# Performance work log

Hardware: AMD Instinct MI355X
Metric: run time of the kernel (lower is better)

The kernel has to match this reference:

```python
import jax, jax.numpy as jnp
import numpy as np

DEPTH = 24
D_MODEL = 384
D_INNER = 768          # expand=2.0
D_STATE = 16
DT_RANK = 24           # ceil(384/16)
D_CONV = 3
PATCH = 16
IMG = 224
N_PATCH = (IMG // PATCH) ** 2  # 196
BATCH = 4


def setup_inputs() -> dict:
    key = jax.random.key(0)
    ks = jax.random.split(key, 12)
    f = lambda k, shape, s=0.02: (jax.random.normal(k, shape) * s).astype(jnp.float32)
    # S4D-real init for A_log, as in mamba
    A_log = jnp.log(jnp.tile(jnp.arange(1, D_STATE + 1, dtype=jnp.float32), (DEPTH, D_INNER, 1)))
    dt_bias = jnp.full((DEPTH, D_INNER), float(np.log(np.expm1(0.01))), dtype=jnp.float32)
    return {
        "z": jax.random.normal(ks[0], (BATCH, 3, IMG, IMG), jnp.float32),
        "x": jax.random.normal(ks[1], (BATCH, 3, IMG, IMG), jnp.float32),
        "patch_W": f(ks[2], (D_MODEL, 3, PATCH, PATCH)),
        "patch_b": jnp.zeros((D_MODEL,), jnp.float32),
        "pos_embed": f(ks[3], (1, N_PATCH + 1, D_MODEL)),
        "norm_w": jnp.ones((DEPTH, D_MODEL), jnp.float32),
        "norm_b": jnp.zeros((DEPTH, D_MODEL), jnp.float32),
        "in_W": f(ks[4], (DEPTH, 2 * D_INNER, D_MODEL)),
        "conv_W": f(ks[5], (DEPTH, D_INNER, D_CONV), 0.2),
        "conv_b": jnp.zeros((DEPTH, D_INNER), jnp.float32),
        "xproj_W": f(ks[6], (DEPTH, DT_RANK + 2 * D_STATE, D_INNER)),
        "dtproj_W": f(ks[7], (DEPTH, D_INNER, DT_RANK), 0.1),
        "dtproj_b": dt_bias,
        "A_log": A_log,
        "D_param": jnp.ones((DEPTH, D_INNER), jnp.float32),
        "out_W": f(ks[8], (DEPTH, D_MODEL, D_INNER)),
        "fnorm_w": jnp.ones((D_MODEL,), jnp.float32),
        "fnorm_b": jnp.zeros((D_MODEL,), jnp.float32),
    }


def _layernorm(x, w, b):
    mu = jnp.mean(x, axis=-1, keepdims=True)
    var = jnp.var(x, axis=-1, keepdims=True)
    return (x - mu) * jax.lax.rsqrt(var + 1e-5) * w + b


def _mixer(x, iw, cw, cb, xw, dw, db, al, dd, ow):
    # x: (B, L, d_model)
    B_, L, _ = x.shape
    xz = jnp.einsum('bld,ed->ble', x, iw)            # (B, L, 2*d_inner)
    xs, zg = jnp.split(xz, 2, axis=-1)
    # depthwise causal conv1d along L (kernel D_CONV)
    xp = jnp.pad(xs, ((0, 0), (D_CONV - 1, 0), (0, 0)))
    xc = cb + sum(xp[:, j:j + L, :] * cw[:, j] for j in range(D_CONV))
    xc = jax.nn.silu(xc)
    dbl = jnp.einsum('bld,ed->ble', xc, xw)          # (B, L, dt_rank + 2*N)
    dt = dbl[..., :DT_RANK]
    Bm = dbl[..., DT_RANK:DT_RANK + D_STATE]         # (B, L, N)
    Cm = dbl[..., DT_RANK + D_STATE:]                # (B, L, N)
    dt = jax.nn.softplus(jnp.einsum('blr,dr->bld', dt, dw) + db)  # (B, L, d_inner)
    A = -jnp.exp(al)                                  # (d_inner, N)
    dA = jnp.exp(dt[..., None] * A)                   # (B, L, d_inner, N)
    dBu = (dt * xc)[..., None] * Bm[:, :, None, :]    # (B, L, d_inner, N)

    def step(h, inp):
        dA_t, dBu_t, C_t = inp
        h = dA_t * h + dBu_t
        return h, jnp.einsum('bdn,bn->bd', h, C_t)

    h0 = jnp.zeros((B_, D_INNER, D_STATE), x.dtype)
    _, ys = jax.lax.scan(step, h0, (dA.transpose(1, 0, 2, 3), dBu.transpose(1, 0, 2, 3), Cm.transpose(1, 0, 2)))
    y = ys.transpose(1, 0, 2) + dd * xc               # (B, L, d_inner)
    y = y * jax.nn.silu(zg)
    return jnp.einsum('ble,de->bld', y, ow)           # (B, L, d_model)


def reference(z, x, patch_W, patch_b, pos_embed, norm_w, norm_b, in_W, conv_W, conv_b,
              xproj_W, dtproj_W, dtproj_b, A_log, D_param, out_W, fnorm_w, fnorm_b):
    def embed(img):
        feat = jax.lax.conv_general_dilated(img, patch_W, (PATCH, PATCH), 'VALID',
                                            dimension_numbers=('NCHW', 'OIHW', 'NCHW'))
        B_, C, H, W = feat.shape
        feat = feat.reshape(B_, C, H * W).transpose(0, 2, 1) + patch_b  # (B, 196, d)
        return feat + pos_embed[:, 1:, :]

    h = jnp.concatenate([embed(z), embed(x)], axis=1)  # (B, 392, d)

    def block(carry, p):
        nw, nb, iw, cw, cb, xw, dw, db, al, dd, ow = p
        y = _layernorm(carry, nw, nb)
        y = _mixer(y, iw, cw, cb, xw, dw, db, al, dd, ow)
        return carry + y, None

    h, _ = jax.lax.scan(block, h, (norm_w, norm_b, in_W, conv_W, conv_b, xproj_W,
                                   dtproj_W, dtproj_b, A_log, D_param, out_W))
    return _layernorm(h, fnorm_w, fnorm_b)
```

## Files before the change

kernel.cpp:

```cpp
#include <hip/hip_runtime.h>

typedef unsigned short u16;
typedef unsigned int   u32;

#define B_     4
#define L_     392
#define T_     1568
#define DM     384
#define DI     768
#define DS     16
#define DTR    24
#define DEPTH_ 24
#define NPATCH 196
#define NC     28
#define CL     14

#define XKC    96
#define XPAD   104
#define OKC    384
#define OPAD   392

typedef __bf16 bf16x8 __attribute__((ext_vector_type(8)));
typedef float  f32x4  __attribute__((ext_vector_type(4)));
typedef u16    u16x4  __attribute__((ext_vector_type(4)));
typedef u16    u16x8  __attribute__((ext_vector_type(8)));

__device__ __forceinline__ u16 f2bf(float f) {
  union { float f; u32 u; } v; v.f = f;
  return (u16)((v.u + 0x7fffu + ((v.u >> 16) & 1u)) >> 16);
}
__device__ __forceinline__ float bf2f(u16 h) {
  union { u32 u; float f; } v; v.u = (u32)h << 16; return v.f;
}

#define RQ0 36864
#define RQ1 1769472
#define RQ2 147456
#define RQ3 884736
#define RQ4 43904
#define RQ_TOT (RQ0+RQ1+RQ2+RQ3+RQ4)

__global__ __launch_bounds__(256) void repack_kernel(
    const float* __restrict__ patchW, u16* __restrict__ pwB,
    const float* __restrict__ inW,    u16* __restrict__ inWb,
    const float* __restrict__ xpW,    u16* __restrict__ xpWb,
    const float* __restrict__ outW,   u16* __restrict__ outWb,
    float* __restrict__ dblz) {
  int i = blockIdx.x * 256 + threadIdx.x;
  const float* sp = nullptr; u16* dp = nullptr;
  if (i < RQ0) {
    int r = i & 15, kb = (i >> 4) % 96, p = i / (16 * 96);
    sp = patchW + (size_t)(p * 16 + r) * 768 + kb * 8;
    dp = pwB + (size_t)i * 8;
  } else { i -= RQ0;
  if (i < RQ1) {
    const int per = 1536 * 48;
    int ly = i / per, rem = i - ly * per;
    int r = rem & 15, kb = (rem >> 4) % 48, p = rem / (16 * 48);
    sp = inW + (size_t)ly * 1536 * 384 + (size_t)(p * 16 + r) * 384 + kb * 8;
    dp = inWb + (size_t)i * 8;
  } else { i -= RQ1;
  if (i < RQ2) {
    const int per = 64 * 96;
    int ly = i / per, rem = i - ly * per;
    int r = rem & 15, kb = (rem >> 4) % 96, p = rem / (16 * 96);
    int row = p * 16 + r;
    dp = xpWb + (size_t)i * 8;
    if (row < 56) {
      sp = xpW + (size_t)ly * 56 * 768 + (size_t)row * 768 + kb * 8;
    } else {
      u16x8 zz = {0,0,0,0,0,0,0,0};
      *(u16x8*)dp = zz;
      return;
    }
  } else { i -= RQ2;
  if (i < RQ3) {
    const int per = 384 * 96;
    int ly = i / per, rem = i - ly * per;
    int r = rem & 15, kb = (rem >> 4) % 96, p = rem / (16 * 96);
    sp = outW + (size_t)ly * 384 * 768 + (size_t)(p * 16 + r) * 768 + kb * 8;
    dp = outWb + (size_t)i * 8;
  } else { i -= RQ3;
  if (i < RQ4) {
    ((float4*)dblz)[i] = make_float4(0.f, 0.f, 0.f, 0.f);
  }
  return; } } } }
  float4 a = *(const float4*)sp;
  float4 b = *(const float4*)(sp + 4);
  u16x8 r8;
  r8[0] = f2bf(a.x); r8[1] = f2bf(a.y); r8[2] = f2bf(a.z); r8[3] = f2bf(a.w);
  r8[4] = f2bf(b.x); r8[5] = f2bf(b.y); r8[6] = f2bf(b.z); r8[7] = f2bf(b.w);
  *(u16x8*)dp = r8;
}

__global__ __launch_bounds__(256) void imcol_kernel(const float* __restrict__ z,
                                                    const float* __restrict__ x,
                                                    u16* __restrict__ out) {
  int idx = blockIdx.x * 256 + threadIdx.x;
  int t = idx / 768, k = idx - t * 768;
  int b = t / L_, l = t - b * L_;
  const float* img = (l < NPATCH) ? z : x;
  int p  = (l < NPATCH) ? l : l - NPATCH;
  int py = p / 14, px = p - py * 14;
  int ic = k >> 8, rem = k & 255, i = rem >> 4, j = rem & 15;
  float v = img[((size_t)b * 3 + ic) * 50176 + (size_t)(py * 16 + i) * 224 + (px * 16 + j)];
  size_t o = ((size_t)(t >> 4) * 96 + (k >> 3)) * 128 + (size_t)(t & 15) * 8 + (k & 7);
  out[o] = f2bf(v);
}

__global__ __launch_bounds__(256) void gemm_patch(const u16* __restrict__ Af,
                                                  const u16* __restrict__ Wf,
                                                  const float* __restrict__ pb,
                                                  const float* __restrict__ pos,
                                                  float* __restrict__ h) {
  int wave = threadIdx.x >> 6, lane = threadIdx.x & 63;
  int r = lane & 15, quad = lane >> 4;
  int t0 = blockIdx.x * 64;
  int p  = blockIdx.y * 4 + wave;
  const u16* wp  = Wf + ((size_t)p * 96 + quad) * 128 + (size_t)r * 8;
  const u16* ap0 = Af + ((size_t)(t0 >> 4) * 96 + quad) * 128 + (size_t)r * 8;

  f32x4 acc[4] = {f32x4{0,0,0,0}, f32x4{0,0,0,0}, f32x4{0,0,0,0}, f32x4{0,0,0,0}};
#pragma unroll
  for (int k0 = 0; k0 < 768; k0 += 32) {
    bf16x8 bfrag = *(const bf16x8*)(wp + (size_t)(k0 >> 3) * 128);
#pragma unroll
    for (int mi = 0; mi < 4; ++mi) {
      bf16x8 afrag = *(const bf16x8*)(ap0 + ((size_t)mi * 96 + (k0 >> 3)) * 128);
      acc[mi] = __builtin_amdgcn_mfma_f32_16x16x32_bf16(afrag, bfrag, acc[mi], 0, 0, 0);
    }
  }
  int ccol = blockIdx.y * 64 + wave * 16 + r;
  float pbv = pb[ccol];
#pragma unroll
  for (int mi = 0; mi < 4; ++mi) {
#pragma unroll
    for (int rr = 0; rr < 4; ++rr) {
      int crow = t0 + mi * 16 + quad * 4 + rr;
      if (crow < T_) {
        int pp = (crow % L_) % NPATCH;
        h[(size_t)crow * DM + ccol] = acc[mi][rr] + pbv + pos[(size_t)(1 + pp) * DM + ccol];
      }
    }
  }
}

__global__ __launch_bounds__(256) void gemm_ln(const float* __restrict__ h,
                                               const float* __restrict__ lw,
                                               const float* __restrict__ lb,
                                               const u16* __restrict__ W3,
                                               u16* __restrict__ xzt) {
  __shared__ u16 atile[64][392];
  int tid = threadIdx.x;
  int w = tid >> 6, l = tid & 63;
  int tok0 = blockIdx.y * 64;

  const int cA = 4 * l;
  const int cB = 256 + 4 * l;
  float4 wA = *(const float4*)(lw + cA);
  float4 bA = *(const float4*)(lb + cA);
  float4 wB = make_float4(0.f, 0.f, 0.f, 0.f), bB = wB;
  if (l < 32) { wB = *(const float4*)(lw + cB); bB = *(const float4*)(lb + cB); }

#pragma unroll 4
  for (int tt = 0; tt < 16; ++tt) {
    int t = w * 16 + tt;
    int tg = tok0 + t; if (tg > T_ - 1) tg = T_ - 1;
    const float* hrow = h + (size_t)tg * DM;
    float4 a = *(const float4*)(hrow + cA);
    float4 b2 = make_float4(0.f, 0.f, 0.f, 0.f);
    if (l < 32) b2 = *(const float4*)(hrow + cB);
    float s  = a.x + a.y + a.z + a.w + b2.x + b2.y + b2.z + b2.w;
    float s2 = a.x * a.x + a.y * a.y + a.z * a.z + a.w * a.w
             + b2.x * b2.x + b2.y * b2.y + b2.z * b2.z + b2.w * b2.w;
#pragma unroll
    for (int o = 32; o; o >>= 1) { s += __shfl_xor(s, o); s2 += __shfl_xor(s2, o); }
    float mu = s * (1.f / DM);
    float rs = rsqrtf(s2 * (1.f / DM) - mu * mu + 1e-5f);
    u16x4 r4;
    r4.x = f2bf((a.x - mu) * rs * wA.x + bA.x);
    r4.y = f2bf((a.y - mu) * rs * wA.y + bA.y);
    r4.z = f2bf((a.z - mu) * rs * wA.z + bA.z);
    r4.w = f2bf((a.w - mu) * rs * wA.w + bA.w);
    *(u16x4*)&atile[t][cA] = r4;
    if (l < 32) {
      u16x4 r4b;
      r4b.x = f2bf((b2.x - mu) * rs * wB.x + bB.x);
      r4b.y = f2bf((b2.y - mu) * rs * wB.y + bB.y);
      r4b.z = f2bf((b2.z - mu) * rs * wB.z + bB.z);
      r4b.w = f2bf((b2.w - mu) * rs * wB.w + bB.w);
      *(u16x4*)&atile[t][cB] = r4b;
    }
  }
  __syncthreads();

  int r = l & 15, u = l >> 4;
  int pbase = blockIdx.x * 4;
  const u16* wp = W3 + ((size_t)pbase * 48 + (size_t)u) * 128 + (size_t)r * 8;
  const u16* lp = &atile[w * 16 + r][u * 8];

  f32x4 acc[4] = {f32x4{0,0,0,0}, f32x4{0,0,0,0}, f32x4{0,0,0,0}, f32x4{0,0,0,0}};
#pragma unroll
  for (int k0 = 0; k0 < DM; k0 += 32) {
    bf16x8 bfrag = *(const bf16x8*)(lp + k0);
#pragma unroll
    for (int mi = 0; mi < 4; ++mi) {
      bf16x8 afrag = *(const bf16x8*)(wp + ((size_t)mi * 48 + (k0 >> 3)) * 128);
      acc[mi] = __builtin_amdgcn_mfma_f32_16x16x32_bf16(afrag, bfrag, acc[mi], 0, 0, 0);
    }
  }
  int ccol = tok0 + w * 16 + r;
  if (ccol < T_) {
#pragma unroll
    for (int mi = 0; mi < 4; ++mi) {
#pragma unroll
      for (int rr2 = 0; rr2 < 4; ++rr2) {
        int crow = pbase * 16 + mi * 16 + u * 4 + rr2;
        xzt[(size_t)crow * T_ + ccol] = f2bf(acc[mi][rr2]);
      }
    }
  }
}

__global__ __launch_bounds__(256) void xproj_conv(const u16* __restrict__ xzt,
                                                  const float* __restrict__ cw,
                                                  const float* __restrict__ cb,
                                                  const u16* __restrict__ Wx3,
                                                  float* __restrict__ dbl) {
  __shared__ u16 tile[64][XPAD];
  int t0 = blockIdx.x * 64;
  int kbeg = blockIdx.z * XKC;
  int tid = threadIdx.x;
  int tl = tid & 63, rq = tid >> 6;
  int t = t0 + tl;
  int tc = (t < T_) ? t : T_ - 1;
  int l = tc % L_;
  for (int kkb = rq * 2; kkb < XKC; kkb += 8) {
    u32 pack = 0;
#pragma unroll
    for (int ss = 0; ss < 2; ++ss) {
      int d = kbeg + kkb + ss;
      const u16* row = xzt + (size_t)d * T_ + tc;
      float acc = cb[d] + cw[d * 3 + 2] * bf2f(row[0]);
      if (l >= 1) acc += cw[d * 3 + 1] * bf2f(row[-1]);
      if (l >= 2) acc += cw[d * 3 + 0] * bf2f(row[-2]);
      float v = acc / (1.f + __expf(-acc));
      pack |= (u32)f2bf(v) << (16 * ss);
    }
    *(u32*)&tile[tl][kkb] = pack;
  }
  __syncthreads();

  int wave = tid >> 6, lane = tid & 63;
  int r = lane & 15, quad = lane >> 4;
  int wcol = wave * 16 + r;
  const u16* wp = Wx3 + ((size_t)wave * 96 + (kbeg >> 3) + quad) * 128 + (size_t)r * 8;

  f32x4 acc4[4] = {f32x4{0,0,0,0}, f32x4{0,0,0,0}, f32x4{0,0,0,0}, f32x4{0,0,0,0}};
#pragma unroll
  for (int k0 = 0; k0 < XKC; k0 += 32) {
    bf16x8 bfrag = *(const bf16x8*)(wp + (size_t)(k0 >> 3) * 128);
#pragma unroll
    for (int mi = 0; mi < 4; ++mi) {
      bf16x8 afrag = *(const bf16x8*)&tile[mi * 16 + r][k0 + quad * 8];
      acc4[mi] = __builtin_amdgcn_mfma_f32_16x16x32_bf16(afrag, bfrag, acc4[mi], 0, 0, 0);
    }
  }
  if (wcol < 56) {
#pragma unroll
    for (int mi = 0; mi < 4; ++mi) {
#pragma unroll
      for (int rr = 0; rr < 4; ++rr) {
        int crow = t0 + mi * 16 + quad * 4 + rr;
        if (crow < T_) atomicAdd(&dbl[(size_t)crow * 56 + wcol], acc4[mi][rr]);
      }
    }
  }
}

__global__ __launch_bounds__(256) void gemm_out(const u16* __restrict__ yt,
                                                const u16* __restrict__ Wo3,
                                                float* __restrict__ h) {
  __shared__ u16 tile[64][OPAD];
  int t0 = blockIdx.x * 64;
  int kbeg = blockIdx.z * OKC;
  int tid = threadIdx.x;
  {
    int tl2 = tid & 31, rq = tid >> 5;
    for (int kk = rq; kk < OKC; kk += 8) {
      int d = kbeg + kk;
      u32 v = *(const u32*)(yt + (size_t)d * T_ + t0 + tl2 * 2);
      tile[tl2 * 2][kk]     = (u16)v;
      tile[tl2 * 2 + 1][kk] = (u16)(v >> 16);
    }
  }
  __syncthreads();

  int wave = tid >> 6, lane = tid & 63;
  int r = lane & 15, quad = lane >> 4;
  int p = blockIdx.y * 4 + wave;
  const u16* wp = Wo3 + ((size_t)p * 96 + (kbeg >> 3) + quad) * 128 + (size_t)r * 8;

  f32x4 acc[4] = {f32x4{0,0,0,0}, f32x4{0,0,0,0}, f32x4{0,0,0,0}, f32x4{0,0,0,0}};
#pragma unroll
  for (int k0 = 0; k0 < OKC; k0 += 32) {
    bf16x8 bfrag = *(const bf16x8*)(wp + (size_t)(k0 >> 3) * 128);
#pragma unroll
    for (int mi = 0; mi < 4; ++mi) {
      bf16x8 afrag = *(const bf16x8*)&tile[mi * 16 + r][k0 + quad * 8];
      acc[mi] = __builtin_amdgcn_mfma_f32_16x16x32_bf16(afrag, bfrag, acc[mi], 0, 0, 0);
    }
  }
  int ccol = blockIdx.y * 64 + wave * 16 + r;
#pragma unroll
  for (int mi = 0; mi < 4; ++mi) {
#pragma unroll
    for (int rr = 0; rr < 4; ++rr) {
      int crow = t0 + mi * 16 + quad * 4 + rr;
      if (crow < T_) atomicAdd(&h[(size_t)crow * DM + ccol], acc[mi][rr]);
    }
  }
}

__global__ __launch_bounds__(384) void ln_kernel(const float* __restrict__ x,
                                                 const float* __restrict__ w,
                                                 const float* __restrict__ b,
                                                 float* __restrict__ out_f) {
  int t = blockIdx.x;
  int i = threadIdx.x;
  float v = x[(size_t)t * DM + i];
  float s = v, s2 = v * v;
#pragma unroll
  for (int o = 32; o; o >>= 1) { s += __shfl_xor(s, o); s2 += __shfl_xor(s2, o); }
  __shared__ float ls[6], ls2[6];
  int wv = i >> 6;
  if ((i & 63) == 0) { ls[wv] = s; ls2[wv] = s2; }
  __syncthreads();
  float ts = 0.f, ts2 = 0.f;
#pragma unroll
  for (int j = 0; j < 6; ++j) { ts += ls[j]; ts2 += ls2[j]; }
  float mu  = ts * (1.f / DM);
  float var = ts2 * (1.f / DM) - mu * mu;
  float rs  = rsqrtf(var + 1e-5f);
  out_f[(size_t)t * DM + i] = (v - mu) * rs * w[i] + b[i];
}

__global__ __launch_bounds__(448) void scan_kernel(const u16* __restrict__ xzt,
                                                   const float* __restrict__ dbl,
                                                   const float* __restrict__ cw,
                                                   const float* __restrict__ cb,
                                                   const float* __restrict__ dtW,
                                                   const float* __restrict__ dtB,
                                                   const float* __restrict__ Alog,
                                                   const float* __restrict__ Dp,
                                                   u16* __restrict__ yt,
                                                   float* __restrict__ dblz) {
  int bd = blockIdx.x;
  int d  = bd % DI;
  int b  = bd / DI;
  int tid = threadIdx.x;
  int n = tid & 15, c = tid >> 4;

  __shared__ float dtsh[L_];
  __shared__ float zsh[L_];
  __shared__ float xcsh[L_];
  __shared__ float Psh[NC][DS], Ssh[NC][DS], Hsh[NC][DS];
  __shared__ float hC[L_][17];

  {
    int i0 = blockIdx.x * 29 + tid;
    if (tid < 29 && i0 < T_ * 56) dblz[i0] = 0.f;
  }

  const float* wr = dtW + (size_t)d * DTR;
  float bias = dtB[d];
  float w0 = cw[d * 3 + 0], w1 = cw[d * 3 + 1], w2 = cw[d * 3 + 2], cbd = cb[d];
  const u16* xrow = xzt + (size_t)d * T_ + b * L_;
  const u16* zrow = xzt + (size_t)(DI + d) * T_ + b * L_;
  if (tid < L_) {
    int l = tid;
    const float* dr = dbl + (size_t)(b * L_ + l) * 56;
    float s = bias;
#pragma unroll
    for (int j = 0; j < DTR; ++j) s += dr[j] * wr[j];
    dtsh[l] = (s > 20.f) ? s : log1pf(__expf(s));
    float zv = bf2f(zrow[l]);
    zsh[l] = zv / (1.f + __expf(-zv));
    float a = cbd + w2 * bf2f(xrow[l]);
    if (l >= 1) a += w1 * bf2f(xrow[l - 1]);
    if (l >= 2) a += w0 * bf2f(xrow[l - 2]);
    xcsh[l] = a / (1.f + __expf(-a));
  }
  float A  = -__expf(Alog[(size_t)d * DS + n]);
  float Dd = Dp[d];
  __syncthreads();

  int tb = b * L_ + c * CL;
  const float* Bp = dbl + (size_t)tb * 56 + DTR + n;
  const float* Cp = Bp + DS;

  float dA[CL], dBu[CL];
  {
    float P = 1.f, S = 0.f;
#pragma unroll
    for (int l = 0; l < CL; ++l) {
      float dtv = dtsh[c * CL + l];
      float xcv = xcsh[c * CL + l];
      float Bv  = Bp[l * 56];
      float e = __expf(dtv * A);
      float u = dtv * xcv * Bv;
      dA[l] = e; dBu[l] = u;
      P *= e;
      S = e * S + u;
    }
    Psh[c][n] = P; Ssh[c][n] = S;
  }
  __syncthreads();
  if (tid < DS) {
    float hh = 0.f;
#pragma unroll
    for (int cc = 0; cc < NC; ++cc) {
      Hsh[cc][tid] = hh;
      hh = Psh[cc][tid] * hh + Ssh[cc][tid];
    }
  }
  __syncthreads();
  {
    float hh = Hsh[c][n];
#pragma unroll
    for (int l = 0; l < CL; ++l) {
      hh = dA[l] * hh + dBu[l];
      hC[c * CL + l][n] = hh * Cp[l * 56];
    }
  }
  __syncthreads();
  if (tid < L_) {
    int l = tid;
    float p = 0.f;
#pragma unroll
    for (int k = 0; k < DS; ++k) p += hC[l][k];
    yt[(size_t)d * T_ + b * L_ + l] = f2bf((p + Dd * xcsh[l]) * zsh[l]);
  }
}

extern "C" void kernel_launch(void* const* d_in, const int* in_sizes, int n_in,
                              void* d_out, int out_size, void* d_ws, size_t ws_size,
                              hipStream_t stream) {
  const float* z      = (const float*)d_in[0];
  const float* x      = (const float*)d_in[1];
  const float* patchW = (const float*)d_in[2];
  const float* patchB = (const float*)d_in[3];
  const float* pos    = (const float*)d_in[4];
  const float* normW  = (const float*)d_in[5];
  const float* normB  = (const float*)d_in[6];
  const float* inW    = (const float*)d_in[7];
  const float* convW  = (const float*)d_in[8];
  const float* convB  = (const float*)d_in[9];
  const float* xprojW = (const float*)d_in[10];
  const float* dtW    = (const float*)d_in[11];
  const float* dtB    = (const float*)d_in[12];
  const float* Alog   = (const float*)d_in[13];
  const float* Dpar   = (const float*)d_in[14];
  const float* outW   = (const float*)d_in[15];
  const float* fnW    = (const float*)d_in[16];
  const float* fnB    = (const float*)d_in[17];
  float* out = (float*)d_out;

  char* base = (char*)d_ws; size_t off = 0;
  auto alloc = [&](size_t bytes) {
    void* p = base + off; off = (off + bytes + 255) & ~(size_t)255; return p;
  };
  float* h    = (float*)alloc((size_t)T_ * DM * 4);
  u16*   xzt  = (u16*)  alloc((size_t)2 * DI * T_ * 2);
  float* dbl  = (float*)alloc((size_t)2 * T_ * 56 * 4);
  u16*   yt   = (u16*)  alloc((size_t)DI * T_ * 2);
  u16*   imcolF=(u16*)  alloc((size_t)100 * 96 * 128 * 2);
  u16*   pwB  = (u16*)  alloc((size_t)DM * 768 * 2);
  u16*   inWb = (u16*)  alloc((size_t)DEPTH_ * 2 * DI * DM * 2);
  u16*   xpWb = (u16*)  alloc((size_t)DEPTH_ * 64 * DI * 2);
  u16*   outWb= (u16*)  alloc((size_t)DEPTH_ * DM * DI * 2);

  repack_kernel<<<dim3((RQ_TOT + 255) / 256), 256, 0, stream>>>(
      patchW, pwB, inW, inWb, xprojW, xpWb, outW, outWb, dbl);

  imcol_kernel<<<dim3(T_ * 768 / 256), 256, 0, stream>>>(z, x, imcolF);
  gemm_patch<<<dim3((T_ + 63) / 64, DM / 64), 256, 0, stream>>>(
      imcolF, pwB, patchB, pos, h);

  const int TG = (T_ + 63) / 64;
  for (int ly = 0; ly < DEPTH_; ++ly) {
    int p = ly & 1;
    float* dblc = dbl + (size_t)p * T_ * 56;
    float* dbln = dbl + (size_t)(p ^ 1) * T_ * 56;
    gemm_ln<<<dim3((2 * DI) / 64, TG), 256, 0, stream>>>(
        h, normW + (size_t)ly * DM, normB + (size_t)ly * DM,
        inWb + (size_t)ly * 2 * DI * DM, xzt);
    xproj_conv<<<dim3(TG, 1, DI / XKC), 256, 0, stream>>>(
        xzt, convW + (size_t)ly * DI * 3, convB + (size_t)ly * DI,
        xpWb + (size_t)ly * 64 * DI, dblc);
    scan_kernel<<<dim3(B_ * DI), 448, 0, stream>>>(
        xzt, dblc, convW + (size_t)ly * DI * 3, convB + (size_t)ly * DI,
        dtW + (size_t)ly * DI * DTR, dtB + (size_t)ly * DI,
        Alog + (size_t)ly * DI * DS, Dpar + (size_t)ly * DI, yt, dbln);
    gemm_out<<<dim3(TG, DM / 64, 2), 256, 0, stream>>>(
        yt, outWb + (size_t)ly * DM * DI, h);
  }

  ln_kernel<<<dim3(T_), dim3(DM), 0, stream>>>(h, fnW, fnB, out);
}
```

Before: 2.060 ms.

## Move dt projection to MFMA kernel and replace out-proj atomics with split partials

Adds a gemm_dt kernel that computes the delta projection plus softplus with bf16 MFMA, writing a transposed dt buffer that the scan reads instead of running a 24-term dot product per thread. gemm_out now writes its two K-split partials to separate buffers instead of using atomicAdd on h. The residual sum is folded into the next layer's LayerNorm load through ping-pong h buffers, and into the final LN. This costs an extra kernel launch per layer, a larger dt buffer, extra partial-sum traffic, and bf16 rounding of the dt inputs.

```diff
diff --git a/kernel.cpp b/kernel.cpp
--- a/kernel.cpp
+++ b/kernel.cpp
@@ -38,13 +38,15 @@
 #define RQ2 147456
 #define RQ3 884736
 #define RQ4 43904
-#define RQ_TOT (RQ0+RQ1+RQ2+RQ3+RQ4)
+#define RQ5 73728
+#define RQ_TOT (RQ0+RQ1+RQ2+RQ3+RQ4+RQ5)
 
 __global__ __launch_bounds__(256) void repack_kernel(
     const float* __restrict__ patchW, u16* __restrict__ pwB,
     const float* __restrict__ inW,    u16* __restrict__ inWb,
     const float* __restrict__ xpW,    u16* __restrict__ xpWb,
     const float* __restrict__ outW,   u16* __restrict__ outWb,
+    const float* __restrict__ dtW,    u16* __restrict__ dtWb,
     float* __restrict__ dblz) {
   int i = blockIdx.x * 256 + threadIdx.x;
   const float* sp = nullptr; u16* dp = nullptr;
@@ -83,8 +85,23 @@
   } else { i -= RQ3;
   if (i < RQ4) {
     ((float4*)dblz)[i] = make_float4(0.f, 0.f, 0.f, 0.f);
-  }
-  return; } } } }
+    return;
+  } else { i -= RQ4;
+  if (i < RQ5) {
+    const int per = 48 * 4 * 16;
+    int ly = i / per, rem = i - ly * per;
+    int p = rem >> 6, rem2 = rem & 63;
+    int kb = rem2 >> 4, r = rem2 & 15;
+    dp = dtWb + (size_t)i * 8;
+    if (kb < 3) {
+      sp = dtW + (size_t)ly * 768 * 24 + (size_t)(p * 16 + r) * 24 + kb * 8;
+    } else {
+      u16x8 zz = {0,0,0,0,0,0,0,0};
+      *(u16x8*)dp = zz;
+      return;
+    }
+  } else return;
+  } } } } }
   float4 a = *(const float4*)sp;
   float4 b = *(const float4*)(sp + 4);
   u16x8 r8;
@@ -145,11 +162,14 @@
   }
 }
 
-__global__ __launch_bounds__(256) void gemm_ln(const float* __restrict__ h,
+__global__ __launch_bounds__(256) void gemm_ln(const float* __restrict__ hin,
+                                               const float* __restrict__ hp,
                                                const float* __restrict__ lw,
                                                const float* __restrict__ lb,
                                                const u16* __restrict__ W3,
-                                               u16* __restrict__ xzt) {
+                                               u16* __restrict__ xzt,
+                                               float* __restrict__ hout,
+                                               int first) {
   __shared__ u16 atile[64][392];
   int tid = threadIdx.x;
   int w = tid >> 6, l = tid & 63;
@@ -166,10 +186,28 @@
   for (int tt = 0; tt < 16; ++tt) {
     int t = w * 16 + tt;
     int tg = tok0 + t; if (tg > T_ - 1) tg = T_ - 1;
-    const float* hrow = h + (size_t)tg * DM;
+    const float* hrow = hin + (size_t)tg * DM;
     float4 a = *(const float4*)(hrow + cA);
     float4 b2 = make_float4(0.f, 0.f, 0.f, 0.f);
     if (l < 32) b2 = *(const float4*)(hrow + cB);
+    if (!first) {
+      const float* p0 = hp + (size_t)tg * DM;
+      const float* p1 = hp + (size_t)(T_ + tg) * DM;
+      float4 q0 = *(const float4*)(p0 + cA);
+      float4 q1 = *(const float4*)(p1 + cA);
+      a.x += q0.x + q1.x; a.y += q0.y + q1.y;
+      a.z += q0.z + q1.z; a.w += q0.w + q1.w;
+      if (l < 32) {
+        float4 s0 = *(const float4*)(p0 + cB);
+        float4 s1 = *(const float4*)(p1 + cB);
+        b2.x += s0.x + s1.x; b2.y += s0.y + s1.y;
+        b2.z += s0.z + s1.z; b2.w += s0.w + s1.w;
+      }
+    }
+    if (blockIdx.x == 0) {
+      *(float4*)(hout + (size_t)tg * DM + cA) = a;
+      if (l < 32) *(float4*)(hout + (size_t)tg * DM + cB) = b2;
+    }
     float s  = a.x + a.y + a.z + a.w + b2.x + b2.y + b2.z + b2.w;
     float s2 = a.x * a.x + a.y * a.y + a.z * a.z + a.w * a.w
              + b2.x * b2.x + b2.y * b2.y + b2.z * b2.z + b2.w * b2.w;
@@ -278,12 +316,62 @@
   }
 }
 
+__global__ __launch_bounds__(256) void gemm_dt(const float* __restrict__ dbl,
+                                               const u16* __restrict__ Wd3,
+                                               const float* __restrict__ dtB,
+                                               float* __restrict__ dtT) {
+  __shared__ u16 btile[64][32];
+  int tid = threadIdx.x;
+  int t0 = blockIdx.y * 64;
+  for (int i = tid; i < 448; i += 256) {
+    if (i < 384) {
+      int row = i / 6, seg = i - row * 6;
+      int tg = t0 + row; if (tg > T_ - 1) tg = T_ - 1;
+      float4 v = *(const float4*)(dbl + (size_t)tg * 56 + seg * 4);
+      u16x4 r4;
+      r4.x = f2bf(v.x); r4.y = f2bf(v.y); r4.z = f2bf(v.z); r4.w = f2bf(v.w);
+      *(u16x4*)&btile[row][seg * 4] = r4;
+    } else {
+      int row = i - 384;
+      u16x8 zz = {0,0,0,0,0,0,0,0};
+      *(u16x8*)&btile[row][24] = zz;
+    }
+  }
+  __syncthreads();
+
+  int w = tid >> 6, l = tid & 63;
+  int r = l & 15, q = l >> 4;
+  int d0 = blockIdx.x * 64;
+  const u16* wp = Wd3 + ((size_t)(d0 >> 4) * 4 + (size_t)q) * 128 + (size_t)r * 8;
+  bf16x8 bfrag = *(const bf16x8*)&btile[w * 16 + r][q * 8];
+
+  f32x4 acc[4] = {f32x4{0,0,0,0}, f32x4{0,0,0,0}, f32x4{0,0,0,0}, f32x4{0,0,0,0}};
+#pragma unroll
+  for (int mi = 0; mi < 4; ++mi) {
+    bf16x8 afrag = *(const bf16x8*)(wp + (size_t)mi * 512);
+    acc[mi] = __builtin_amdgcn_mfma_f32_16x16x32_bf16(afrag, bfrag, acc[mi], 0, 0, 0);
+  }
+  int t = t0 + w * 16 + r;
+  if (t < T_) {
+#pragma unroll
+    for (int mi = 0; mi < 4; ++mi) {
+#pragma unroll
+      for (int rr = 0; rr < 4; ++rr) {
+        int d = d0 + mi * 16 + q * 4 + rr;
+        float s = acc[mi][rr] + dtB[d];
+        dtT[(size_t)d * T_ + t] = (s > 20.f) ? s : log1pf(__expf(s));
+      }
+    }
+  }
+}
+
 __global__ __launch_bounds__(256) void gemm_out(const u16* __restrict__ yt,
                                                 const u16* __restrict__ Wo3,
-                                                float* __restrict__ h) {
+                                                float* __restrict__ hpart) {
   __shared__ u16 tile[64][OPAD];
   int t0 = blockIdx.x * 64;
   int kbeg = blockIdx.z * OKC;
+  float* hp = hpart + (size_t)blockIdx.z * T_ * DM;
   int tid = threadIdx.x;
   {
     int tl2 = tid & 31, rq = tid >> 5;
@@ -317,18 +405,20 @@
 #pragma unroll
     for (int rr = 0; rr < 4; ++rr) {
       int crow = t0 + mi * 16 + quad * 4 + rr;
-      if (crow < T_) atomicAdd(&h[(size_t)crow * DM + ccol], acc[mi][rr]);
+      if (crow < T_) hp[(size_t)crow * DM + ccol] = acc[mi][rr];
     }
   }
 }
 
 __global__ __launch_bounds__(384) void ln_kernel(const float* __restrict__ x,
+                                                 const float* __restrict__ hp,
                                                  const float* __restrict__ w,
                                                  const float* __restrict__ b,
                                                  float* __restrict__ out_f) {
   int t = blockIdx.x;
   int i = threadIdx.x;
-  float v = x[(size_t)t * DM + i];
+  size_t idx = (size_t)t * DM + i;
+  float v = x[idx] + hp[idx] + hp[(size_t)T_ * DM + idx];
   float s = v, s2 = v * v;
 #pragma unroll
   for (int o = 32; o; o >>= 1) { s += __shfl_xor(s, o); s2 += __shfl_xor(s2, o); }
@@ -342,15 +432,14 @@
   float mu  = ts * (1.f / DM);
   float var = ts2 * (1.f / DM) - mu * mu;
   float rs  = rsqrtf(var + 1e-5f);
-  out_f[(size_t)t * DM + i] = (v - mu) * rs * w[i] + b[i];
+  out_f[idx] = (v - mu) * rs * w[i] + b[i];
 }
 
 __global__ __launch_bounds__(448) void scan_kernel(const u16* __restrict__ xzt,
                                                    const float* __restrict__ dbl,
                                                    const float* __restrict__ cw,
                                                    const float* __restrict__ cb,
-                                                   const float* __restrict__ dtW,
-                                                   const float* __restrict__ dtB,
+                                                   const float* __restrict__ dtT,
                                                    const float* __restrict__ Alog,
                                                    const float* __restrict__ Dp,
                                                    u16* __restrict__ yt,
@@ -372,18 +461,12 @@
     if (tid < 29 && i0 < T_ * 56) dblz[i0] = 0.f;
   }
 
-  const float* wr = dtW + (size_t)d * DTR;
-  float bias = dtB[d];
   float w0 = cw[d * 3 + 0], w1 = cw[d * 3 + 1], w2 = cw[d * 3 + 2], cbd = cb[d];
   const u16* xrow = xzt + (size_t)d * T_ + b * L_;
   const u16* zrow = xzt + (size_t)(DI + d) * T_ + b * L_;
   if (tid < L_) {
     int l = tid;
-    const float* dr = dbl + (size_t)(b * L_ + l) * 56;
-    float s = bias;
-#pragma unroll
-    for (int j = 0; j < DTR; ++j) s += dr[j] * wr[j];
-    dtsh[l] = (s > 20.f) ? s : log1pf(__expf(s));
+    dtsh[l] = dtT[(size_t)d * T_ + b * L_ + l];
     float zv = bf2f(zrow[l]);
     zsh[l] = zv / (1.f + __expf(-zv));
     float a = cbd + w2 * bf2f(xrow[l]);
@@ -470,41 +553,48 @@
   auto alloc = [&](size_t bytes) {
     void* p = base + off; off = (off + bytes + 255) & ~(size_t)255; return p;
   };
-  float* h    = (float*)alloc((size_t)T_ * DM * 4);
+  float* hA   = (float*)alloc((size_t)T_ * DM * 4);
+  float* hB   = (float*)alloc((size_t)T_ * DM * 4);
+  float* hpart= (float*)alloc((size_t)2 * T_ * DM * 4);
   u16*   xzt  = (u16*)  alloc((size_t)2 * DI * T_ * 2);
   float* dbl  = (float*)alloc((size_t)2 * T_ * 56 * 4);
+  float* dtT  = (float*)alloc((size_t)DI * T_ * 4);
   u16*   yt   = (u16*)  alloc((size_t)DI * T_ * 2);
   u16*   imcolF=(u16*)  alloc((size_t)100 * 96 * 128 * 2);
   u16*   pwB  = (u16*)  alloc((size_t)DM * 768 * 2);
   u16*   inWb = (u16*)  alloc((size_t)DEPTH_ * 2 * DI * DM * 2);
   u16*   xpWb = (u16*)  alloc((size_t)DEPTH_ * 64 * DI * 2);
   u16*   outWb= (u16*)  alloc((size_t)DEPTH_ * DM * DI * 2);
+  u16*   dtWb = (u16*)  alloc((size_t)DEPTH_ * DI * 32 * 2);
 
   repack_kernel<<<dim3((RQ_TOT + 255) / 256), 256, 0, stream>>>(
-      patchW, pwB, inW, inWb, xprojW, xpWb, outW, outWb, dbl);
+      patchW, pwB, inW, inWb, xprojW, xpWb, outW, outWb, dtW, dtWb, dbl);
 
   imcol_kernel<<<dim3(T_ * 768 / 256), 256, 0, stream>>>(z, x, imcolF);
   gemm_patch<<<dim3((T_ + 63) / 64, DM / 64), 256, 0, stream>>>(
-      imcolF, pwB, patchB, pos, h);
+      imcolF, pwB, patchB, pos, hA);
 
   const int TG = (T_ + 63) / 64;
   for (int ly = 0; ly < DEPTH_; ++ly) {
     int p = ly & 1;
+    const float* hin = p ? hB : hA;
+    float*       hout= p ? hA : hB;
     float* dblc = dbl + (size_t)p * T_ * 56;
     float* dbln = dbl + (size_t)(p ^ 1) * T_ * 56;
     gemm_ln<<<dim3((2 * DI) / 64, TG), 256, 0, stream>>>(
-        h, normW + (size_t)ly * DM, normB + (size_t)ly * DM,
-        inWb + (size_t)ly * 2 * DI * DM, xzt);
+        hin, hpart, normW + (size_t)ly * DM, normB + (size_t)ly * DM,
+        inWb + (size_t)ly * 2 * DI * DM, xzt, hout, ly == 0 ? 1 : 0);
     xproj_conv<<<dim3(TG, 1, DI / XKC), 256, 0, stream>>>(
         xzt, convW + (size_t)ly * DI * 3, convB + (size_t)ly * DI,
         xpWb + (size_t)ly * 64 * DI, dblc);
+    gemm_dt<<<dim3(DI / 64, TG), 256, 0, stream>>>(
+        dblc, dtWb + (size_t)ly * DI * 32, dtB + (size_t)ly * DI, dtT);
     scan_kernel<<<dim3(B_ * DI), 448, 0, stream>>>(
         xzt, dblc, convW + (size_t)ly * DI * 3, convB + (size_t)ly * DI,
-        dtW + (size_t)ly * DI * DTR, dtB + (size_t)ly * DI,
-        Alog + (size_t)ly * DI * DS, Dpar + (size_t)ly * DI, yt, dbln);
+        dtT, Alog + (size_t)ly * DI * DS, Dpar + (size_t)ly * DI, yt, dbln);
     gemm_out<<<dim3(TG, DM / 64, 2), 256, 0, stream>>>(
-        yt, outWb + (size_t)ly * DM * DI, h);
-  }
-
-  ln_kernel<<<dim3(T_), dim3(DM), 0, stream>>>(h, fnW, fnB, out);
-}
+        yt, outWb + (size_t)ly * DM * DI, hpart);
+  }
+
+  ln_kernel<<<dim3(T_), dim3(DM), 0, stream>>>(hA, hpart, fnW, fnB, out);
+}
```

Result: slower. 2.226 ms (+8.1%).
